# Optimization experiments

Measured on AMD Instinct MI355X. Metric: run time of the kernel, lower is better.

## Reference

```python
import jax, jax.numpy as jnp
import numpy as np

B, N, S = 8, 4096, 1024
D1, D2 = 128, 256
IN_CH, OUT_CH = D1 + D2, 256
BN_EPS = 1e-5


def setup_inputs() -> dict:
    key = jax.random.key(0)
    ks = jax.random.split(key, 12)
    inp = {
        "xyz1": jax.random.normal(ks[0], (B, N, 3), jnp.float32),
        "xyz2": jax.random.normal(ks[1], (B, S, 3), jnp.float32),
        "points1": jax.random.normal(ks[2], (B, N, D1), jnp.float32),
        "points2": jax.random.normal(ks[3], (B, S, D2), jnp.float32),
        # fuse: Conv1d(in_ch->out_ch, k=1) + BN
        "W_fuse": jax.random.normal(ks[4], (OUT_CH, IN_CH), jnp.float32) * (1.0 / np.sqrt(IN_CH)),
        "b_fuse": jnp.zeros((OUT_CH,), jnp.float32),
        "g_fuse": jnp.ones((OUT_CH,), jnp.float32),
        "bt_fuse": jnp.zeros((OUT_CH,), jnp.float32),
        # res block net1: Conv1d(out_ch->out_ch) + BN (res_expansion=1.0)
        "W1": jax.random.normal(ks[5], (OUT_CH, OUT_CH), jnp.float32) * (1.0 / np.sqrt(OUT_CH)),
        "b1": jnp.zeros((OUT_CH,), jnp.float32),
        "g1": jnp.ones((OUT_CH,), jnp.float32),
        "bt1": jnp.zeros((OUT_CH,), jnp.float32),
        # res block net2: Conv1d(out_ch->out_ch) + BN
        "W2": jax.random.normal(ks[6], (OUT_CH, OUT_CH), jnp.float32) * (1.0 / np.sqrt(OUT_CH)),
        "b2": jnp.zeros((OUT_CH,), jnp.float32),
        "g2": jnp.ones((OUT_CH,), jnp.float32),
        "bt2": jnp.zeros((OUT_CH,), jnp.float32),
    }
    return inp


def _bn(x, g, b):
    # BatchNorm1d training-mode forward: stats over (batch, length), x: [B, C, L]
    m = jnp.mean(x, axis=(0, 2), keepdims=True)
    v = jnp.var(x, axis=(0, 2), keepdims=True)
    return (x - m) * jax.lax.rsqrt(v + BN_EPS) * g[None, :, None] + b[None, :, None]


def _conv1x1(x, W, b):
    # x: [B, C_in, L], W: [C_out, C_in] -> [B, C_out, L]
    return jnp.einsum("oc,bcl->bol", W, x) + b[None, :, None]


def _gelu(x):
    return jax.nn.gelu(x, approximate=False)  # torch nn.GELU default (erf)


def reference(xyz1, xyz2, points1, points2,
              W_fuse, b_fuse, g_fuse, bt_fuse,
              W1, b1, g1, bt1, W2, b2, g2, bt2):
    # squared pairwise distances [B, N, S] without B x N x S x 3 intermediate
    d = (jnp.sum(xyz1 * xyz1, -1)[:, :, None]
         - 2.0 * jnp.einsum("bnc,bsc->bns", xyz1, xyz2)
         + jnp.sum(xyz2 * xyz2, -1)[:, None, :])
    # 3 nearest coarse points per dense point (== sort ascending, take first 3)
    neg_d3, idx = jax.lax.top_k(-d, 3)            # [B, N, 3]
    d3 = -neg_d3
    recip = 1.0 / (d3 + 1e-8)
    w = recip / jnp.sum(recip, axis=2, keepdims=True)  # [B, N, 3]
    gathered = points2[jnp.arange(points2.shape[0])[:, None, None], idx]  # [B, N, 3, D2]
    interp = jnp.sum(gathered * w[..., None], axis=2)  # [B, N, D2]

    new_points = jnp.concatenate([points1, interp], axis=-1)  # [B, N, D1+D2]
    x = jnp.transpose(new_points, (0, 2, 1))                   # [B, C, N]

    # fuse: conv-bn-gelu
    x = _gelu(_bn(_conv1x1(x, W_fuse, b_fuse), g_fuse, bt_fuse))
    # residual block: gelu(bn(conv(gelu(bn(conv(x))))) + x)
    y = _gelu(_bn(_conv1x1(x, W1, b1), g1, bt1))
    y = _bn(_conv1x1(y, W2, b2), g2, bt2)
    x = _gelu(y + x)

    return jnp.transpose(x, (0, 2, 1))  # [B, N, out_ch]
```

## Files before the change

### kernel.cpp

```cpp
#include <hip/hip_runtime.h>
#include <hip/hip_bf16.h>

constexpr int Bb = 8, Nn = 4096, Ss = 1024;
constexpr int D1 = 128, D2 = 256, KIN = 384, OC = 256;
constexpr int L = Bb * Nn;
constexpr float BN_EPS = 1e-5f;

typedef __attribute__((ext_vector_type(4))) float floatx4;
typedef __attribute__((ext_vector_type(8))) __bf16 bf16x8;

#define DEV __device__ __forceinline__

DEV float bf2f(unsigned short u) {
    union { unsigned int i; float f; } v; v.i = ((unsigned int)u) << 16; return v.f;
}
DEV unsigned short f2bf(float f) {
    union { float f; unsigned int i; } v; v.f = f;
    unsigned int x = v.i;
    return (unsigned short)((x + 0x7FFFu + ((x >> 16) & 1u)) >> 16);
}
DEV float gelu_f(float x) {
    float u = x * (0.7978845608f + 0.0356774081f * x * x);
    float t = __expf(-2.0f * u);
    return x * __builtin_amdgcn_rcpf(1.0f + t);
}

DEV bool probe_isf(const unsigned int* __restrict__ w, int tid) {
    unsigned int lo = w[tid & 63] & 0xFFFFu;
    int e = (int)((lo >> 7) & 0xFF);
    unsigned long long m = __ballot(e >= 100 && e <= 144);
    return __popcll(m) < 48;
}

DEV void merge3(float& d0, float& d1, float& d2, int& i0, int& i1, int& i2,
                float e0, float e1, float e2, int j0, int j1, int j2, bool pref) {
    float a0 = d0, a1 = d1, a2 = d2; int x0 = i0, x1 = i1, x2 = i2;
    float b0 = e0, b1 = e1;          int y0 = j0, y1 = j1;
    bool t = pref ? (a0 <= b0) : (a0 < b0);
    d0 = t ? a0 : b0; i0 = t ? x0 : y0;
    a0 = t ? a1 : a0; x0 = t ? x1 : x0;
    a1 = t ? a2 : a1; x1 = t ? x2 : x1;
    b0 = t ? b0 : b1; y0 = t ? y0 : y1;
    b1 = t ? b1 : e2; y1 = t ? y1 : j2;
    t = pref ? (a0 <= b0) : (a0 < b0);
    d1 = t ? a0 : b0; i1 = t ? x0 : y0;
    a0 = t ? a1 : a0; x0 = t ? x1 : x0;
    b0 = t ? b0 : b1; y0 = t ? y0 : y1;
    t = pref ? (a0 <= b0) : (a0 < b0);
    d2 = t ? a0 : b0; i2 = t ? x0 : y0;
}

__global__ __launch_bounds__(256) void k_front(const void* __restrict__ xyz1_,
                                               const void* __restrict__ xyz2_,
                                               const void* __restrict__ w0_,
                                               const void* __restrict__ w1_,
                                               const void* __restrict__ w2_,
                                               unsigned short* __restrict__ Wdst,
                                               float* __restrict__ stats,
                                               int* __restrict__ dflag,
                                               int* __restrict__ nn_idx,
                                               float* __restrict__ nn_w) {
    int tid = threadIdx.x;
    int bid = blockIdx.x;
    bool isf = probe_isf((const unsigned int*)xyz1_, tid);

    if (bid < 6) {
        stats[bid * 256 + tid] = 0.0f;
        if (bid == 0 && tid == 0) *dflag = isf ? 1 : 0;
        return;
    }
    if (bid < 902) {
        int i = (bid - 6) * 256 + tid;
        const void* src; int off;
        if (i < 98304)       { src = w0_; off = i; }
        else if (i < 163840) { src = w1_; off = i - 98304; }
        else                 { src = w2_; off = i - 163840; }
        Wdst[i] = isf ? f2bf(((const float*)src)[off]) : ((const unsigned short*)src)[off];
        return;
    }

    __shared__ alignas(16) float s4[Ss * 4 + 32];
    int bn0 = (bid - 902) * 32;
    int b = bn0 >> 12;

    if (isf) {
        const float* p2 = (const float*)xyz2_ + (size_t)b * Ss * 3;
        for (int i = tid; i < Ss * 3; i += 256) {
            int s = i / 3, k = i - s * 3;
            s4[s * 4 + k + ((s >> 7) << 2)] = p2[i];
        }
    } else {
        const unsigned short* p2 = (const unsigned short*)xyz2_ + (size_t)b * Ss * 3;
        for (int i = tid; i < Ss * 3; i += 256) {
            int s = i / 3, k = i - s * 3;
            s4[s * 4 + k + ((s >> 7) << 2)] = bf2f(p2[i]);
        }
    }
    __syncthreads();
    for (int s = tid; s < Ss; s += 256) {
        int a = s * 4 + ((s >> 7) << 2);
        float x = s4[a], y = s4[a + 1], z = s4[a + 2];
        s4[a + 3] = x * x + y * y + z * z;
    }
    __syncthreads();

    int part = tid & 7;
    int bn = bn0 + (tid >> 3);
    float x1, y1, z1;
    if (isf) {
        const float* p1 = (const float*)xyz1_ + (size_t)bn * 3;
        x1 = p1[0]; y1 = p1[1]; z1 = p1[2];
    } else {
        const unsigned short* p1 = (const unsigned short*)xyz1_ + (size_t)bn * 3;
        x1 = bf2f(p1[0]); y1 = bf2f(p1[1]); z1 = bf2f(p1[2]);
    }
    float n1 = x1 * x1 + y1 * y1 + z1 * z1;

    float d0 = 3.4e38f, d1 = 3.4e38f, d2 = 3.4e38f;
    int i0 = 0, i1 = 0, i2 = 0;
    const float* sp = &s4[part * 516];
#pragma unroll 4
    for (int j = 0; j < 128; ++j) {
        float4 qv = *(const float4*)(sp + j * 4);
        float d = n1 + qv.w - 2.0f * (x1 * qv.x + y1 * qv.y + z1 * qv.z);
        int s = part * 128 + j;
        bool c2 = d < d2, c1 = d < d1, c0 = d < d0;
        d2 = c1 ? d1 : (c2 ? d : d2); i2 = c1 ? i1 : (c2 ? s : i2);
        d1 = c0 ? d0 : (c1 ? d : d1); i1 = c0 ? i0 : (c1 ? s : i1);
        d0 = c0 ? d  : d0;            i0 = c0 ? s  : i0;
    }
#pragma unroll
    for (int m = 1; m <= 4; m <<= 1) {
        float e0 = __shfl_xor(d0, m, 64), e1 = __shfl_xor(d1, m, 64), e2 = __shfl_xor(d2, m, 64);
        int   j0 = __shfl_xor(i0, m, 64), j1 = __shfl_xor(i1, m, 64), j2 = __shfl_xor(i2, m, 64);
        bool pref = (part < (part ^ m));
        merge3(d0, d1, d2, i0, i1, i2, e0, e1, e2, j0, j1, j2, pref);
    }
    if (part == 0) {
        float r0 = 1.0f / (d0 + 1e-8f), r1 = 1.0f / (d1 + 1e-8f), r2 = 1.0f / (d2 + 1e-8f);
        float rs = 1.0f / (r0 + r1 + r2);
        nn_idx[bn * 3 + 0] = i0; nn_idx[bn * 3 + 1] = i1; nn_idx[bn * 3 + 2] = i2;
        nn_w[bn * 3 + 0] = r0 * rs; nn_w[bn * 3 + 1] = r1 * rs; nn_w[bn * 3 + 2] = r2 * rs;
    }
}

__global__ __launch_bounds__(256) void k_gemm1(const void* __restrict__ p1_,
                                               const void* __restrict__ p2_,
                                               const int* __restrict__ nn_idx,
                                               const float* __restrict__ nn_w,
                                               const int* __restrict__ dflag,
                                               const unsigned short* __restrict__ W,
                                               unsigned short* __restrict__ Out,
                                               float* __restrict__ S1, float* __restrict__ S2) {
    __shared__ alignas(16) unsigned short As[64 * 64];
    __shared__ alignas(16) unsigned short Bs[256 * 64];
    __shared__ float sS1[256], sS2[256];

    int tid = threadIdx.x;
    int l0 = blockIdx.x * 64;
    int wn = tid >> 6, lane = tid & 63, quad = lane >> 4, lr = lane & 15;
    bool isf = (*dflag != 0);

    floatx4 acc[4][4];
#pragma unroll
    for (int mi = 0; mi < 4; ++mi)
#pragma unroll
        for (int ni = 0; ni < 4; ++ni) acc[mi][ni] = (floatx4){0.f, 0.f, 0.f, 0.f};

    for (int kc = 0; kc < KIN / 64; ++kc) {
        __syncthreads();
#pragma unroll
        for (int it = 0; it < 2; ++it) {
            int idx = it * 256 + tid, row = idx >> 3, c8 = idx & 7;
            int pt = l0 + row;
            int c0 = kc * 64 + c8 * 8;
            union { uint4 v; unsigned short u[8]; } va;
            if (c0 < D1) {
                if (isf) {
                    const float* p = (const float*)p1_ + (size_t)pt * D1 + c0;
                    float4 f0 = *(const float4*)p;
                    float4 f1 = *(const float4*)(p + 4);
                    va.u[0] = f2bf(f0.x); va.u[1] = f2bf(f0.y); va.u[2] = f2bf(f0.z); va.u[3] = f2bf(f0.w);
                    va.u[4] = f2bf(f1.x); va.u[5] = f2bf(f1.y); va.u[6] = f2bf(f1.z); va.u[7] = f2bf(f1.w);
                } else {
                    va.v = *(const uint4*)((const unsigned short*)p1_ + (size_t)pt * D1 + c0);
                }
            } else {
                int c2 = c0 - D1;
                int b = pt >> 12;
                int j0 = nn_idx[pt * 3], j1 = nn_idx[pt * 3 + 1], j2 = nn_idx[pt * 3 + 2];
                float w0 = nn_w[pt * 3], w1 = nn_w[pt * 3 + 1], w2 = nn_w[pt * 3 + 2];
                if (isf) {
                    const float* base = (const float*)p2_;
                    const float* r0 = base + ((size_t)(b * Ss + j0)) * D2 + c2;
                    const float* r1 = base + ((size_t)(b * Ss + j1)) * D2 + c2;
                    const float* r2 = base + ((size_t)(b * Ss + j2)) * D2 + c2;
#pragma unroll
                    for (int h = 0; h < 2; ++h) {
                        float4 a0 = *(const float4*)(r0 + h * 4);
                        float4 a1 = *(const float4*)(r1 + h * 4);
                        float4 a2 = *(const float4*)(r2 + h * 4);
                        va.u[h * 4 + 0] = f2bf(w0 * a0.x + w1 * a1.x + w2 * a2.x);
                        va.u[h * 4 + 1] = f2bf(w0 * a0.y + w1 * a1.y + w2 * a2.y);
                        va.u[h * 4 + 2] = f2bf(w0 * a0.z + w1 * a1.z + w2 * a2.z);
                        va.u[h * 4 + 3] = f2bf(w0 * a0.w + w1 * a1.w + w2 * a2.w);
                    }
                } else {
                    const unsigned short* base = (const unsigned short*)p2_;
                    uint4 v0 = *(const uint4*)(base + ((size_t)(b * Ss + j0)) * D2 + c2);
                    uint4 v1 = *(const uint4*)(base + ((size_t)(b * Ss + j1)) * D2 + c2);
                    uint4 v2 = *(const uint4*)(base + ((size_t)(b * Ss + j2)) * D2 + c2);
                    const unsigned short* u0 = (const unsigned short*)&v0;
                    const unsigned short* u1 = (const unsigned short*)&v1;
                    const unsigned short* u2 = (const unsigned short*)&v2;
#pragma unroll
                    for (int j = 0; j < 8; ++j)
                        va.u[j] = f2bf(w0 * bf2f(u0[j]) + w1 * bf2f(u1[j]) + w2 * bf2f(u2[j]));
                }
            }
            *(uint4*)&As[row * 64 + ((c8 ^ (row & 7)) << 3)] = va.v;
        }
#pragma unroll
        for (int it = 0; it < 8; ++it) {
            int idx = it * 256 + tid, row = idx >> 3, c8 = idx & 7;
            uint4 vb = *(const uint4*)(W + (size_t)row * KIN + kc * 64 + c8 * 8);
            *(uint4*)&Bs[row * 64 + ((c8 ^ (row & 7)) << 3)] = vb;
        }
        __syncthreads();
#pragma unroll
        for (int ks8 = 0; ks8 < 2; ++ks8) {
            bf16x8 af[4], bfr[4];
#pragma unroll
            for (int mi = 0; mi < 4; ++mi) {
                int ra = mi * 16 + lr;
                af[mi] = *(const bf16x8*)&As[ra * 64 + ((((ks8 << 2) + quad) ^ (ra & 7)) << 3)];
            }
#pragma unroll
            for (int ni = 0; ni < 4; ++ni) {
                int rb = wn * 64 + ni * 16 + lr;
                bfr[ni] = *(const bf16x8*)&Bs[rb * 64 + ((((ks8 << 2) + quad) ^ (rb & 7)) << 3)];
            }
#pragma unroll
            for (int mi = 0; mi < 4; ++mi)
#pragma unroll
                for (int ni = 0; ni < 4; ++ni)
                    acc[mi][ni] = __builtin_amdgcn_mfma_f32_16x16x32_bf16(af[mi], bfr[ni], acc[mi][ni], 0, 0, 0);
        }
    }

    float p1a[4] = {0, 0, 0, 0}, p2a[4] = {0, 0, 0, 0};
#pragma unroll
    for (int mi = 0; mi < 4; ++mi)
#pragma unroll
        for (int ni = 0; ni < 4; ++ni)
#pragma unroll
            for (int r = 0; r < 4; ++r) {
                float v = acc[mi][ni][r];
                int row = l0 + mi * 16 + quad * 4 + r;
                int col = wn * 64 + ni * 16 + lr;
                Out[(size_t)row * OC + col] = f2bf(v);
                p1a[ni] += v; p2a[ni] += v * v;
            }
    sS1[tid] = 0.f; sS2[tid] = 0.f;
    __syncthreads();
#pragma unroll
    for (int ni = 0; ni < 4; ++ni) {
        atomicAdd(&sS1[wn * 64 + ni * 16 + lr], p1a[ni]);
        atomicAdd(&sS2[wn * 64 + ni * 16 + lr], p2a[ni]);
    }
    __syncthreads();
    atomicAdd(&S1[tid], sS1[tid]);
    atomicAdd(&S2[tid], sS2[tid]);
}

template <int K>
__global__ __launch_bounds__(256) void k_gemm(const unsigned short* __restrict__ A,
                                              const unsigned short* __restrict__ W,
                                              unsigned short* __restrict__ Out,
                                              float* __restrict__ S1, float* __restrict__ S2,
                                              const float* __restrict__ S1in,
                                              const float* __restrict__ S2in,
                                              const void* __restrict__ g_,
                                              const void* __restrict__ bt_,
                                              const int* __restrict__ dflag) {
    __shared__ alignas(16) unsigned short As[64 * 64];
    __shared__ alignas(16) unsigned short Bs[256 * 64];
    __shared__ float sS1[256], sS2[256];
    __shared__ float sCA[256], sCC[256];

    int tid = threadIdx.x;
    int l0 = blockIdx.x * 64;
    int wn = tid >> 6, lane = tid & 63, quad = lane >> 4, lr = lane & 15;

    {
        float m = S1in[tid] * (1.0f / (float)L);
        float var = S2in[tid] * (1.0f / (float)L) - m * m;
        float g, bt;
        if (*dflag) { g = ((const float*)g_)[tid]; bt = ((const float*)bt_)[tid]; }
        else { g = bf2f(((const unsigned short*)g_)[tid]); bt = bf2f(((const unsigned short*)bt_)[tid]); }
        float a = g * rsqrtf(var + BN_EPS);
        sCA[tid] = a;
        sCC[tid] = bt - m * a;
    }

    floatx4 acc[4][4];
#pragma unroll
    for (int mi = 0; mi < 4; ++mi)
#pragma unroll
        for (int ni = 0; ni < 4; ++ni) acc[mi][ni] = (floatx4){0.f, 0.f, 0.f, 0.f};

    constexpr int KC = K / 64;
    for (int kc = 0; kc < KC; ++kc) {
        __syncthreads();
#pragma unroll
        for (int it = 0; it < 2; ++it) {
            int idx = it * 256 + tid, row = idx >> 3, c8 = idx & 7;
            union { uint4 v; unsigned short u[8]; } va;
            va.v = *(const uint4*)(A + (size_t)(l0 + row) * K + kc * 64 + c8 * 8);
            int kb = kc * 64 + c8 * 8;
#pragma unroll
            for (int j = 0; j < 8; ++j) {
                float f = bf2f(va.u[j]);
                va.u[j] = f2bf(gelu_f(sCA[kb + j] * f + sCC[kb + j]));
            }
            *(uint4*)&As[row * 64 + ((c8 ^ (row & 7)) << 3)] = va.v;
        }
#pragma unroll
        for (int it = 0; it < 8; ++it) {
            int idx = it * 256 + tid, row = idx >> 3, c8 = idx & 7;
            uint4 vb = *(const uint4*)(W + (size_t)row * K + kc * 64 + c8 * 8);
            *(uint4*)&Bs[row * 64 + ((c8 ^ (row & 7)) << 3)] = vb;
        }
        __syncthreads();
#pragma unroll
        for (int ks8 = 0; ks8 < 2; ++ks8) {
            bf16x8 af[4], bfr[4];
#pragma unroll
            for (int mi = 0; mi < 4; ++mi) {
                int ra = mi * 16 + lr;
                af[mi] = *(const bf16x8*)&As[ra * 64 + ((((ks8 << 2) + quad) ^ (ra & 7)) << 3)];
            }
#pragma unroll
            for (int ni = 0; ni < 4; ++ni) {
                int rb = wn * 64 + ni * 16 + lr;
                bfr[ni] = *(const bf16x8*)&Bs[rb * 64 + ((((ks8 << 2) + quad) ^ (rb & 7)) << 3)];
            }
#pragma unroll
            for (int mi = 0; mi < 4; ++mi)
#pragma unroll
                for (int ni = 0; ni < 4; ++ni)
                    acc[mi][ni] = __builtin_amdgcn_mfma_f32_16x16x32_bf16(af[mi], bfr[ni], acc[mi][ni], 0, 0, 0);
        }
    }

    float p1a[4] = {0, 0, 0, 0}, p2a[4] = {0, 0, 0, 0};
#pragma unroll
    for (int mi = 0; mi < 4; ++mi)
#pragma unroll
        for (int ni = 0; ni < 4; ++ni)
#pragma unroll
            for (int r = 0; r < 4; ++r) {
                float v = acc[mi][ni][r];
                int row = l0 + mi * 16 + quad * 4 + r;
                int col = wn * 64 + ni * 16 + lr;
                Out[(size_t)row * OC + col] = f2bf(v);
                p1a[ni] += v; p2a[ni] += v * v;
            }
    sS1[tid] = 0.f; sS2[tid] = 0.f;
    __syncthreads();
#pragma unroll
    for (int ni = 0; ni < 4; ++ni) {
        atomicAdd(&sS1[wn * 64 + ni * 16 + lr], p1a[ni]);
        atomicAdd(&sS2[wn * 64 + ni * 16 + lr], p2a[ni]);
    }
    __syncthreads();
    atomicAdd(&S1[tid], sS1[tid]);
    atomicAdd(&S2[tid], sS2[tid]);
}

__global__ __launch_bounds__(256) void k_final(const unsigned short* __restrict__ t0,
                                               const unsigned short* __restrict__ t2,
                                               const float* __restrict__ S1_0, const float* __restrict__ S2_0,
                                               const float* __restrict__ S1_2, const float* __restrict__ S2_2,
                                               const void* __restrict__ g0_, const void* __restrict__ bt0_,
                                               const void* __restrict__ g2_, const void* __restrict__ bt2_,
                                               const int* __restrict__ dflag,
                                               void* __restrict__ out_) {
    __shared__ float sA0[256], sC0[256], sA2[256], sC2[256];
    int tid = threadIdx.x;
    bool isf = (*dflag != 0);
    {
        float m0 = S1_0[tid] * (1.0f / (float)L);
        float v0_ = S2_0[tid] * (1.0f / (float)L) - m0 * m0;
        float m2 = S1_2[tid] * (1.0f / (float)L);
        float v2_ = S2_2[tid] * (1.0f / (float)L) - m2 * m2;
        float g0, b0, g2, b2;
        if (isf) {
            g0 = ((const float*)g0_)[tid]; b0 = ((const float*)bt0_)[tid];
            g2 = ((const float*)g2_)[tid]; b2 = ((const float*)bt2_)[tid];
        } else {
            g0 = bf2f(((const unsigned short*)g0_)[tid]); b0 = bf2f(((const unsigned short*)bt0_)[tid]);
            g2 = bf2f(((const unsigned short*)g2_)[tid]); b2 = bf2f(((const unsigned short*)bt2_)[tid]);
        }
        float a0 = g0 * rsqrtf(v0_ + BN_EPS);
        float a2 = g2 * rsqrtf(v2_ + BN_EPS);
        sA0[tid] = a0; sC0[tid] = b0 - m0 * a0;
        sA2[tid] = a2; sC2[tid] = b2 - m2 * a2;
    }
    __syncthreads();

    int idx = (blockIdx.x * 256 + tid) * 8;
    int col = idx & (OC - 1);
    union { uint4 v; unsigned short u[8]; } v0, v2;
    v0.v = *(const uint4*)(t0 + idx);
    v2.v = *(const uint4*)(t2 + idx);
    float r[8];
#pragma unroll
    for (int j = 0; j < 8; ++j) {
        float x = gelu_f(sA0[col + j] * bf2f(v0.u[j]) + sC0[col + j]);
        float y = sA2[col + j] * bf2f(v2.u[j]) + sC2[col + j];
        r[j] = gelu_f(x + y);
    }
    if (isf) {
        float* o = (float*)out_ + idx;
        float4 lo = {r[0], r[1], r[2], r[3]};
        float4 hi = {r[4], r[5], r[6], r[7]};
        *(float4*)o = lo;
        *(float4*)(o + 4) = hi;
    } else {
        union { uint4 v; unsigned short u[8]; } vo;
#pragma unroll
        for (int j = 0; j < 8; ++j) vo.u[j] = f2bf(r[j]);
        *(uint4*)((unsigned short*)out_ + idx) = vo.v;
    }
}

extern "C" void kernel_launch(void* const* d_in, const int* in_sizes, int n_in,
                              void* d_out, int out_size, void* d_ws, size_t ws_size,
                              hipStream_t stream) {
    const void* xyz1    = d_in[0];
    const void* xyz2    = d_in[1];
    const void* points1 = d_in[2];
    const void* points2 = d_in[3];
    const void* W_fuse  = d_in[4];
    const void* g_fuse  = d_in[6];
    const void* bt_fuse = d_in[7];
    const void* W1      = d_in[8];
    const void* g1      = d_in[10];
    const void* bt1     = d_in[11];
    const void* W2      = d_in[12];
    const void* g2      = d_in[14];
    const void* bt2     = d_in[15];

    char* ws = (char*)d_ws;
    unsigned short* t2 = (unsigned short*)ws;
    unsigned short* t0 = (unsigned short*)(ws + 25165824);
    unsigned short* t1 = (unsigned short*)d_out;
    int*   nn_idx = (int*)(ws + 41943040);
    float* nn_w   = (float*)(ws + 42336256);
    float* stats  = (float*)(ws + 42729472);
    int*   dflag  = (int*)(ws + 42729472 + 3072 * 4);
    unsigned short* Wbf = (unsigned short*)(ws + 42745856);

    float *S1_0 = stats,        *S2_0 = stats + 256;
    float *S1_1 = stats + 512,  *S2_1 = stats + 768;
    float *S1_2 = stats + 1024, *S2_2 = stats + 1280;

    k_front<<<1926, 256, 0, stream>>>(xyz1, xyz2, W_fuse, W1, W2, Wbf, stats, dflag, nn_idx, nn_w);
    k_gemm1<<<L / 64, 256, 0, stream>>>(points1, points2, nn_idx, nn_w, dflag,
                                        Wbf, t0, S1_0, S2_0);
    k_gemm<OC><<<L / 64, 256, 0, stream>>>(t0, Wbf + 98304, t1, S1_1, S2_1,
                                           S1_0, S2_0, g_fuse, bt_fuse, dflag);
    k_gemm<OC><<<L / 64, 256, 0, stream>>>(t1, Wbf + 163840, t2, S1_2, S2_2,
                                           S1_1, S2_1, g1, bt1, dflag);
    k_final<<<L * OC / (256 * 8), 256, 0, stream>>>(t0, t2, S1_0, S2_0, S1_2, S2_2,
                                                    g_fuse, bt_fuse, g2, bt2, dflag, d_out);
}
```

Measured before the change: 231.5 us.

## Load weight tiles directly into LDS and stage full A tile once

The weights are pre-permuted in the conversion kernel into the XOR-swizzled layout, so B tiles can be copied with global_load_lds straight into shared memory without passing through registers. In k_gemm the whole 64xK activation tile, with BN and GELU applied, is now staged into LDS once before the K loop instead of once per K chunk. This is meant to cut register traffic and shorten the per-iteration load phase. In exchange, LDS use grows with K, which may lower occupancy.

```diff
diff --git a/kernel.cpp b/kernel.cpp
--- a/kernel.cpp
+++ b/kernel.cpp
@@ -30,6 +30,12 @@
     int e = (int)((lo >> 7) & 0xFF);
     unsigned long long m = __ballot(e >= 100 && e <= 144);
     return __popcll(m) < 48;
+}
+
+template <int K> DEV int permoff(int off) {
+    int row = off / K, rr = off - row * K;
+    int cg = (rr >> 3) & 7;
+    return row * K + (rr & ~63) + (((cg ^ (row & 7)) << 3)) + (rr & 7);
 }
 
 DEV void merge3(float& d0, float& d1, float& d2, int& i0, int& i1, int& i2,
@@ -72,9 +78,9 @@
     if (bid < 902) {
         int i = (bid - 6) * 256 + tid;
         const void* src; int off;
-        if (i < 98304)       { src = w0_; off = i; }
-        else if (i < 163840) { src = w1_; off = i - 98304; }
-        else                 { src = w2_; off = i - 163840; }
+        if (i < 98304)       { src = w0_; off = permoff<384>(i); }
+        else if (i < 163840) { src = w1_; off = permoff<256>(i - 98304); }
+        else                 { src = w2_; off = permoff<256>(i - 163840); }
         Wdst[i] = isf ? f2bf(((const float*)src)[off]) : ((const unsigned short*)src)[off];
         return;
     }
@@ -169,6 +175,17 @@
 
     for (int kc = 0; kc < KIN / 64; ++kc) {
         __syncthreads();
+#pragma unroll
+        for (int it = 0; it < 8; ++it) {
+            int chunk = it * 4 + wn;
+            int row = chunk * 8 + (lane >> 3);
+            int cg = lane & 7;
+            const unsigned short* src = W + (size_t)row * KIN + kc * 64 + cg * 8;
+            __builtin_amdgcn_global_load_lds(
+                (const __attribute__((address_space(1))) void*)src,
+                (__attribute__((address_space(3))) void*)&Bs[chunk * 512],
+                16, 0, 0);
+        }
 #pragma unroll
         for (int it = 0; it < 2; ++it) {
             int idx = it * 256 + tid, row = idx >> 3, c8 = idx & 7;
@@ -220,12 +237,6 @@
             }
             *(uint4*)&As[row * 64 + ((c8 ^ (row & 7)) << 3)] = va.v;
         }
-#pragma unroll
-        for (int it = 0; it < 8; ++it) {
-            int idx = it * 256 + tid, row = idx >> 3, c8 = idx & 7;
-            uint4 vb = *(const uint4*)(W + (size_t)row * KIN + kc * 64 + c8 * 8);
-            *(uint4*)&Bs[row * 64 + ((c8 ^ (row & 7)) << 3)] = vb;
-        }
         __syncthreads();
 #pragma unroll
         for (int ks8 = 0; ks8 < 2; ++ks8) {
@@ -283,7 +294,7 @@
                                               const void* __restrict__ g_,
                                               const void* __restrict__ bt_,
                                               const int* __restrict__ dflag) {
-    __shared__ alignas(16) unsigned short As[64 * 64];
+    __shared__ alignas(16) unsigned short As[64 * K];
     __shared__ alignas(16) unsigned short Bs[256 * 64];
     __shared__ float sS1[256], sS2[256];
     __shared__ float sCA[256], sCC[256];
@@ -302,6 +313,23 @@
         sCA[tid] = a;
         sCC[tid] = bt - m * a;
     }
+    __syncthreads();
+
+#pragma unroll
+    for (int it = 0; it < (64 * K / 8) / 256; ++it) {
+        int idx = it * 256 + tid;
+        int row = idx >> 5, cg = idx & 31;
+        union { uint4 v; unsigned short u[8]; } va;
+        va.v = *(const uint4*)(A + (size_t)(l0 + row) * K + cg * 8);
+        int kb = cg * 8;
+#pragma unroll
+        for (int j = 0; j < 8; ++j) {
+            float f = bf2f(va.u[j]);
+            va.u[j] = f2bf(gelu_f(sCA[kb + j] * f + sCC[kb + j]));
+        }
+        int sg = (cg & 24) | ((cg & 7) ^ (row & 7));
+        *(uint4*)&As[row * K + sg * 8] = va.v;
+    }
 
     floatx4 acc[4][4];
 #pragma unroll
@@ -313,23 +341,15 @@
     for (int kc = 0; kc < KC; ++kc) {
         __syncthreads();
 #pragma unroll
-        for (int it = 0; it < 2; ++it) {
-            int idx = it * 256 + tid, row = idx >> 3, c8 = idx & 7;
-            union { uint4 v; unsigned short u[8]; } va;
-            va.v = *(const uint4*)(A + (size_t)(l0 + row) * K + kc * 64 + c8 * 8);
-            int kb = kc * 64 + c8 * 8;
-#pragma unroll
-            for (int j = 0; j < 8; ++j) {
-                float f = bf2f(va.u[j]);
-                va.u[j] = f2bf(gelu_f(sCA[kb + j] * f + sCC[kb + j]));
-            }
-            *(uint4*)&As[row * 64 + ((c8 ^ (row & 7)) << 3)] = va.v;
-        }
-#pragma unroll
         for (int it = 0; it < 8; ++it) {
-            int idx = it * 256 + tid, row = idx >> 3, c8 = idx & 7;
-            uint4 vb = *(const uint4*)(W + (size_t)row * K + kc * 64 + c8 * 8);
-            *(uint4*)&Bs[row * 64 + ((c8 ^ (row & 7)) << 3)] = vb;
+            int chunk = it * 4 + wn;
+            int row = chunk * 8 + (lane >> 3);
+            int cg = lane & 7;
+            const unsigned short* src = W + (size_t)row * K + kc * 64 + cg * 8;
+            __builtin_amdgcn_global_load_lds(
+                (const __attribute__((address_space(1))) void*)src,
+                (__attribute__((address_space(3))) void*)&Bs[chunk * 512],
+                16, 0, 0);
         }
         __syncthreads();
 #pragma unroll
@@ -338,7 +358,8 @@
 #pragma unroll
             for (int mi = 0; mi < 4; ++mi) {
                 int ra = mi * 16 + lr;
-                af[mi] = *(const bf16x8*)&As[ra * 64 + ((((ks8 << 2) + quad) ^ (ra & 7)) << 3)];
+                int g = kc * 8 + ((((ks8 << 2) + quad)) ^ (ra & 7));
+                af[mi] = *(const bf16x8*)&As[ra * K + g * 8];
             }
 #pragma unroll
             for (int ni = 0; ni < 4; ++ni) {
```

Measured after the change: 229.1 us. About the same (-1.0%).
